# Kernel optimization log

Hardware: AMD Instinct MI355X
Metric: run time of the kernel (lower is better)

The kernel has to match this reference:

```python
import jax, jax.numpy as jnp
import numpy as np
import math

B, H, L, DK, D, LOCAL = 4, 8, 2048, 64, 512, 4


def setup_inputs() -> dict:
    key = jax.random.key(0)
    ks = jax.random.split(key, 9)
    n = L
    return {
        'query': jax.random.normal(ks[0], (B, H, L, DK), jnp.float32),
        'key': jax.random.normal(ks[1], (B, H, L, DK), jnp.float32),
        'value': jax.random.normal(ks[2], (B, H, L, DK), jnp.float32),
        'users': jax.random.normal(ks[3], (B, L, D), jnp.float32),
        'mask': jnp.tril(jnp.ones((L, L), dtype=bool))[None, None],  # causal [1,1,L,L]
        'rel_pos_w': jax.random.normal(ks[4], (2 * n - 1, DK * LOCAL), jnp.float32) * 0.02,
        'user_proj_w': jax.random.normal(ks[5], (DK * LOCAL, D), jnp.float32) * 0.02,
        'user_proj_b': jax.random.normal(ks[6], (DK * LOCAL,), jnp.float32) * 0.02,
        'mlp_w': jax.random.normal(ks[7], (LOCAL, DK), jnp.float32) * 0.1,
        'mlp_b': jax.random.normal(ks[8], (LOCAL,), jnp.float32) * 0.1,
    }


def reference(query, key, value, users, mask, rel_pos_w, user_proj_w, user_proj_b, mlp_w, mlp_b):
    b, h, l, dk = query.shape
    local = mlp_w.shape[0]
    g = h - local
    n = l
    scale = 1.0 / math.sqrt(dk)
    NEG = -1e12  # MAX_VAL in the torch source

    # ---- global heads: plain softmax attention ----
    qg, kg, vg = query[:, :g], key[:, :g], value[:, :g]
    sg = jnp.einsum('bhqd,bhkd->bhqk', qg, kg) * scale
    sg = jnp.where(mask, sg, NEG)
    pg = jax.nn.softmax(sg, axis=-1)
    og = jnp.einsum('bhqk,bhkd->bhqd', pg, vg)

    # ---- local (LOCKER) heads ----
    ql, kl, vl = query[:, g:], key[:, g:], value[:, g:]
    sl = jnp.einsum('bhqd,bhkd->bhqk', ql, kl) * scale

    # reweight = Linear(d_k,1)(rel_pos + v_q + v_k + user_proj(users)_q) per local head.
    # Linear over a sum decomposes exactly (same math, avoids [b,local,l,l,dk] tensor):
    rel_tab = rel_pos_w.reshape(2 * n - 1, local, dk)
    rel_scores = jnp.einsum('rhd,hd->rh', rel_tab, mlp_w)          # [2n-1, local]
    pos = jnp.arange(n)
    distance = pos[None, :] - pos[:, None] + n - 1                  # [l, l]
    rel_term = rel_scores[distance].transpose(2, 0, 1)              # [local, l, l]

    v_term = jnp.einsum('bhkd,hd->bhk', vl, mlp_w)                  # [b, local, l]
    u = (users @ user_proj_w.T + user_proj_b).reshape(b, l, local, dk)
    u_term = jnp.einsum('bqhd,hd->bhq', u, mlp_w)                   # [b, local, l]

    reweight = (rel_term[None]
                + v_term[:, :, None, :]      # value_l.unsqueeze(-3): varies over key idx
                + v_term[:, :, :, None]      # value_l.unsqueeze(-2): varies over query idx
                + u_term[:, :, :, None]      # user term broadcast over key idx
                + mlp_b[None, :, None, None])

    sl = sl + reweight
    sl = jnp.where(mask, sl, NEG)
    pl = jax.nn.softmax(sl, axis=-1)
    ol = jnp.einsum('bhqk,bhkd->bhqd', pl, vl)

    return jnp.concatenate([og, ol], axis=1)  # [b, h, l, d_k]
```

## Files before the change

### kernel.cpp

```cpp
#include <hip/hip_runtime.h>

#define TL 2048
#define NHEAD 8
#define NLOC 4
#define L2E 1.44269504f

typedef __attribute__((ext_vector_type(4))) float f32x4;
typedef __attribute__((ext_vector_type(8))) __bf16 bf16x8;
typedef __attribute__((ext_vector_type(4))) __bf16 bf16x4;
typedef __attribute__((ext_vector_type(8))) unsigned short u16x8;

static __device__ __forceinline__ unsigned short f2bf(float f) {
    unsigned u = __float_as_uint(f);
    u = (u + 0x7FFFu + ((u >> 16) & 1u)) >> 16;
    return (unsigned short)u;
}
static __device__ __forceinline__ float bf2f(unsigned short u) {
    return __uint_as_float(((unsigned)u) << 16);
}
static __device__ __forceinline__ void gl_lds16(const void* g, void* l) {
    __builtin_amdgcn_global_load_lds(
        (const __attribute__((address_space(1))) void*)g,
        (__attribute__((address_space(3))) void*)l, 16, 0, 0);
}

__global__ __launch_bounds__(256) void relscore_kernel(
    const float* __restrict__ rel_pos_w, const float* __restrict__ mlp_w,
    unsigned short* __restrict__ rel_sb) {
    int r = blockIdx.x;
    int t = threadIdx.x;
    int w = t >> 6, lane = t & 63;
    float v = rel_pos_w[r * 256 + t] * mlp_w[t];
#pragma unroll
    for (int off = 32; off; off >>= 1) v += __shfl_xor(v, off);
    if (lane == 0) rel_sb[w * 4096 + r] = f2bf(v * L2E);
}

__global__ __launch_bounds__(256) void preconv_kernel(
    const float* __restrict__ key, const float* __restrict__ value,
    const float* __restrict__ mlp_w,
    unsigned short* __restrict__ Kb, unsigned short* __restrict__ Vtb,
    unsigned short* __restrict__ vtb) {
    __shared__ float Vf[64][66];
    int blk = blockIdx.x;
    int t = threadIdx.x;
    int bh = blk >> 5, kt = blk & 31;
    int h = bh & 7, b = bh >> 3;
    size_t src = (size_t)blk * 4096;
    size_t dst = (size_t)blk * 4096;

#pragma unroll
    for (int i = 0; i < 2; ++i) {
        int ch = t + i * 256;
        int row = ch >> 3, c = ch & 7;
        const float* kp = key + src + row * 64 + c * 8;
        f32x4 a = *(const f32x4*)kp;
        f32x4 bb = *(const f32x4*)(kp + 4);
        u16x8 o;
#pragma unroll
        for (int j = 0; j < 4; ++j) { o[j] = f2bf(a[j]); o[4 + j] = f2bf(bb[j]); }
        *(u16x8*)&Kb[dst + row * 64 + ((c ^ (row & 7)) << 3)] = o;
    }
    {
        int row = t >> 2, q4 = t & 3;
        const float* vp = value + src + row * 64 + q4 * 16;
#pragma unroll
        for (int j = 0; j < 4; ++j)
            *(f32x4*)&Vf[row][q4 * 16 + j * 4] = *(const f32x4*)(vp + j * 4);
    }
    __syncthreads();
#pragma unroll
    for (int i = 0; i < 2; ++i) {
        int ch = t + i * 256;
        int dr = ch >> 3, c = ch & 7;
        u16x8 o;
#pragma unroll
        for (int j = 0; j < 8; ++j) o[j] = f2bf(Vf[c * 8 + j][dr]);
        *(u16x8*)&Vtb[dst + dr * 64 + ((c ^ (dr & 7)) << 3)] = o;
    }
    if (h >= NLOC) {
        int wave = t >> 6, lane = t & 63;
        float mw = mlp_w[(h - NLOC) * 64 + lane];
        unsigned short* vout = vtb + (size_t)((b * NLOC + h - NLOC) * TL) + kt * 64;
#pragma unroll
        for (int i = 0; i < 16; ++i) {
            int row = wave * 16 + i;
            float v = Vf[row][lane] * mw;
#pragma unroll
            for (int off = 32; off; off >>= 1) v += __shfl_xor(v, off);
            if (lane == 0) vout[row] = f2bf(v * L2E);
        }
    }
}

__global__ __launch_bounds__(256, 4) void attn_kernel(
    const float* __restrict__ query,
    const unsigned short* __restrict__ Kb, const unsigned short* __restrict__ Vtb,
    const unsigned short* __restrict__ rel_sb, const unsigned short* __restrict__ vtb,
    float* __restrict__ out) {

    __shared__ __align__(16) unsigned char smem[37248];
    unsigned short* Ks0  = (unsigned short*)smem;
    unsigned short* Vt0  = (unsigned short*)(smem + 16384);
    unsigned short* relb = (unsigned short*)(smem + 32768);
    unsigned short* bias0 = (unsigned short*)(smem + 36992);

    int bid = blockIdx.x;
    int qbi = bid >> 5;
    int bh = bid & 31;
    int qb = (qbi < 16) ? (31 - qbi) : (qbi - 16);
    int h = bh & 7;
    int b = bh >> 3;
    int q0 = qb << 6;
    int t = threadIdx.x;
    int wave = t >> 6, lane = t & 63;
    int l15 = lane & 15, l4 = lane >> 4;
    bool islocal = (h >= NLOC);

    size_t base = (size_t)bh * TL * 64;
    const unsigned short* Ktiles = Kb + (size_t)bh * 32 * 4096;
    const unsigned short* Vtiles = Vtb + (size_t)bh * 32 * 4096;
    const unsigned short* vtp =
        vtb + (islocal ? (size_t)((b * NLOC + h - NLOC) * TL) : 0);

    gl_lds16(Ktiles + t * 8, Ks0 + t * 8);
    gl_lds16(Ktiles + 2048 + t * 8, Ks0 + 2048 + t * 8);
    gl_lds16(Vtiles + t * 8, Vt0 + t * 8);
    gl_lds16(Vtiles + 2048 + t * 8, Vt0 + 2048 + t * 8);
    if (islocal) {
        const u16x8* src = (const u16x8*)(rel_sb + (h - NLOC) * 4096);
        u16x8* dst = (u16x8*)relb;
        dst[t] = src[t];
        if (t < 8) {
            dst[256 + t] = src[256 + t];
            *(u16x8*)&bias0[t * 8] = *(const u16x8*)&vtp[t * 8];
        }
    }

    int qt = q0 + wave * 16;
    int q = qt + l15;

    const float SC = 0.125f * L2E;
    bf16x8 qf0, qf1;
    {
        const float* qsrc = query + base + (size_t)q * 64 + l4 * 8;
        f32x4 a = *(const f32x4*)qsrc;
        f32x4 bb = *(const f32x4*)(qsrc + 4);
        f32x4 c = *(const f32x4*)(qsrc + 32);
        f32x4 d = *(const f32x4*)(qsrc + 36);
        u16x8 u0, u1;
#pragma unroll
        for (int j = 0; j < 4; ++j) {
            u0[j] = f2bf(a[j] * SC); u0[4 + j] = f2bf(bb[j] * SC);
            u1[j] = f2bf(c[j] * SC); u1[4 + j] = f2bf(d[j] * SC);
        }
        qf0 = __builtin_bit_cast(bf16x8, u0);
        qf1 = __builtin_bit_cast(bf16x8, u1);
    }

    float m = -1e30f, lsum = 0.0f;
    f32x4 acc0 = {0.f, 0.f, 0.f, 0.f};
    f32x4 acc1 = acc0, acc2 = acc0, acc3 = acc0;

    __syncthreads();

    int cur = 0;
    for (int kt = 0; kt <= qb; ++kt) {
        unsigned short* Ks = Ks0 + cur * 4096;
        unsigned short* Vt = Vt0 + cur * 4096;
        unsigned short* bias = bias0 + cur * 64;

        if (kt < qb) {
            int nb = cur ^ 1;
            const unsigned short* gk = Ktiles + (size_t)(kt + 1) * 4096;
            const unsigned short* gv = Vtiles + (size_t)(kt + 1) * 4096;
            gl_lds16(gk + t * 8, Ks0 + nb * 4096 + t * 8);
            gl_lds16(gk + 2048 + t * 8, Ks0 + nb * 4096 + 2048 + t * 8);
            gl_lds16(gv + t * 8, Vt0 + nb * 4096 + t * 8);
            gl_lds16(gv + 2048 + t * 8, Vt0 + nb * 4096 + 2048 + t * 8);
            if (islocal && t < 8)
                *(u16x8*)&bias0[nb * 64 + t * 8] =
                    *(const u16x8*)&vtp[(kt + 1) * 64 + t * 8];
        }

        int k0 = kt << 6;
        bool diag = (kt == qb);
        int s16max = diag ? wave : 3;

        f32x4 sfr[4];
#pragma unroll
        for (int s16 = 0; s16 < 4; ++s16) {
            if (s16 <= s16max) {
                int r = s16 * 16 + l15;
                int sw = r & 7;
                const bf16x8 kf0 = *(const bf16x8*)&Ks[r * 64 + ((l4 ^ sw) << 3)];
                const bf16x8 kf1 = *(const bf16x8*)&Ks[r * 64 + (((4 + l4) ^ sw) << 3)];
                f32x4 z = {0.f, 0.f, 0.f, 0.f};
                z = __builtin_amdgcn_mfma_f32_16x16x32_bf16(kf0, qf0, z, 0, 0, 0);
                z = __builtin_amdgcn_mfma_f32_16x16x32_bf16(kf1, qf1, z, 0, 0, 0);
                sfr[s16] = z;
            } else {
                sfr[s16] = (f32x4){-1e30f, -1e30f, -1e30f, -1e30f};
            }
        }

        float sv[16];
        float tmax = -1e30f;
#pragma unroll
        for (int s16 = 0; s16 < 4; ++s16) {
#pragma unroll
            for (int rg = 0; rg < 4; ++rg) {
                int kk = s16 * 16 + l4 * 4 + rg;
                int k = k0 + kk;
                float s = sfr[s16][rg];
                if (s16 <= s16max) {
                    if (islocal) s += bf2f(relb[k - q + 2047]) + bf2f(bias[kk]);
                    if (diag && k > q) s = -1e30f;
                }
                sv[s16 * 4 + rg] = s;
                tmax = fmaxf(tmax, s);
            }
        }
        tmax = fmaxf(tmax, __shfl_xor(tmax, 16));
        tmax = fmaxf(tmax, __shfl_xor(tmax, 32));
        if (__any(tmax > m + 11.5f)) {
            float newm = fmaxf(m, tmax);
            float corr = exp2f(m - newm);
            lsum *= corr;
            acc0 *= corr; acc1 *= corr; acc2 *= corr; acc3 *= corr;
            m = newm;
        }
        float psum = 0.f;
        bf16x4 pq[4];
#pragma unroll
        for (int s16 = 0; s16 < 4; ++s16) {
#pragma unroll
            for (int rg = 0; rg < 4; ++rg) {
                float p = exp2f(sv[s16 * 4 + rg] - m);
                psum += p;
                pq[s16][rg] = (__bf16)p;
            }
        }
        psum += __shfl_xor(psum, 16);
        psum += __shfl_xor(psum, 32);
        lsum += psum;

        asm volatile("s_waitcnt lgkmcnt(0)" ::: "memory");
        __builtin_amdgcn_s_barrier();
        __builtin_amdgcn_sched_barrier(0);

        unsigned short* Pw = Ks + wave * 1024;
#pragma unroll
        for (int s16 = 0; s16 < 4; ++s16) {
            int c = 2 * s16 + (l4 >> 1);
            *(unsigned long long*)&Pw[l15 * 64 + ((c ^ (l15 & 7)) << 3) + ((l4 & 1) << 2)] =
                __builtin_bit_cast(unsigned long long, pq[s16]);
        }

#pragma unroll
        for (int half = 0; half < 2; ++half) {
            const bf16x8 pf =
                *(const bf16x8*)&Pw[l15 * 64 + (((half * 4 + l4) ^ (l15 & 7)) << 3)];
            int cbase = half * 4 + l4;
#pragma unroll
            for (int dblk = 0; dblk < 4; ++dblk) {
                int r = dblk * 16 + l15;
                const bf16x8 vf =
                    *(const bf16x8*)&Vt[r * 64 + ((cbase ^ (r & 7)) << 3)];
                f32x4* ac = dblk == 0 ? &acc0 : dblk == 1 ? &acc1
                          : dblk == 2 ? &acc2 : &acc3;
                *ac = __builtin_amdgcn_mfma_f32_16x16x32_bf16(vf, pf, *ac, 0, 0, 0);
            }
        }

        __syncthreads();
        cur ^= 1;
    }

    float invl = 1.0f / lsum;
    float* ob = (float*)(smem + wave * 4352);
    *(f32x4*)&ob[l15 * 68 + 0  + l4 * 4] = acc0 * invl;
    *(f32x4*)&ob[l15 * 68 + 16 + l4 * 4] = acc1 * invl;
    *(f32x4*)&ob[l15 * 68 + 32 + l4 * 4] = acc2 * invl;
    *(f32x4*)&ob[l15 * 68 + 48 + l4 * 4] = acc3 * invl;
    size_t obase = base + (size_t)qt * 64;
#pragma unroll
    for (int it = 0; it < 4; ++it) {
        int row = lane >> 2;
        int col = (lane & 3) * 16 + it * 4;
        f32x4 o = *(const f32x4*)&ob[row * 68 + col];
        *(f32x4*)(out + obase + (size_t)row * 64 + col) = o;
    }
}

extern "C" void kernel_launch(void* const* d_in, const int* in_sizes, int n_in,
                              void* d_out, int out_size, void* d_ws, size_t ws_size,
                              hipStream_t stream) {
    const float* query = (const float*)d_in[0];
    const float* key = (const float*)d_in[1];
    const float* value = (const float*)d_in[2];
    const float* rel_pos_w = (const float*)d_in[5];
    const float* mlp_w = (const float*)d_in[8];
    float* out = (float*)d_out;

    unsigned short* Kb = (unsigned short*)d_ws;
    unsigned short* Vtb = Kb + 32 * 32 * 4096;
    unsigned short* rel_sb = Vtb + 32 * 32 * 4096;
    unsigned short* vtb = rel_sb + 4 * 4096;

    relscore_kernel<<<4095, 256, 0, stream>>>(rel_pos_w, mlp_w, rel_sb);
    preconv_kernel<<<1024, 256, 0, stream>>>(key, value, mlp_w, Kb, Vtb, vtb);
    attn_kernel<<<1024, 256, 0, stream>>>(query, Kb, Vtb, rel_sb, vtb, out);
}
```

Measured before the change: 88.95 us.

## Pair causal query blocks per workgroup and keep relative bias in fp32

Each workgroup now handles two query blocks (qb and 31-qb) of the same batch-head back to back, so every block runs 33 key tiles and the causal work is balanced. The grid is halved to 512 and the flash-attention state is flushed and reset between the two blocks. Relative-position scores and the per-key value bias are now stored in LDS as fp32 instead of bf16, which raises LDS use and lowers the occupancy hint to 2. The intent is to remove the causal load imbalance and the tail effect of the old grid, at the cost of fewer resident workgroups and more LDS per block.

```diff
diff --git a/kernel.cpp b/kernel.cpp
--- a/kernel.cpp
+++ b/kernel.cpp
@@ -26,14 +26,14 @@
 
 __global__ __launch_bounds__(256) void relscore_kernel(
     const float* __restrict__ rel_pos_w, const float* __restrict__ mlp_w,
-    unsigned short* __restrict__ rel_sb) {
+    float* __restrict__ rel_sf) {
     int r = blockIdx.x;
     int t = threadIdx.x;
     int w = t >> 6, lane = t & 63;
     float v = rel_pos_w[r * 256 + t] * mlp_w[t];
 #pragma unroll
     for (int off = 32; off; off >>= 1) v += __shfl_xor(v, off);
-    if (lane == 0) rel_sb[w * 4096 + r] = f2bf(v * L2E);
+    if (lane == 0) rel_sf[w * 4096 + r] = v * L2E;
 }
 
 __global__ __launch_bounds__(256) void preconv_kernel(
@@ -93,25 +93,25 @@
     }
 }
 
-__global__ __launch_bounds__(256, 4) void attn_kernel(
+__global__ __launch_bounds__(256, 2) void attn_kernel(
     const float* __restrict__ query,
     const unsigned short* __restrict__ Kb, const unsigned short* __restrict__ Vtb,
-    const unsigned short* __restrict__ rel_sb, const unsigned short* __restrict__ vtb,
+    const float* __restrict__ rel_sf, const unsigned short* __restrict__ vtb,
     float* __restrict__ out) {
 
-    __shared__ __align__(16) unsigned char smem[37248];
-    unsigned short* Ks0  = (unsigned short*)smem;
-    unsigned short* Vt0  = (unsigned short*)(smem + 16384);
-    unsigned short* relb = (unsigned short*)(smem + 32768);
-    unsigned short* bias0 = (unsigned short*)(smem + 36992);
+    __shared__ __align__(16) unsigned char smem[59136];
+    unsigned short* Ks0 = (unsigned short*)smem;
+    unsigned short* Vt0 = (unsigned short*)(smem + 16384);
+    float* relf  = (float*)(smem + 32768);
+    float* biasf = (float*)(smem + 41216);
+    float* epil  = (float*)(smem + 41728);
 
     int bid = blockIdx.x;
-    int qbi = bid >> 5;
-    int bh = bid & 31;
-    int qb = (qbi < 16) ? (31 - qbi) : (qbi - 16);
-    int h = bh & 7;
-    int b = bh >> 3;
-    int q0 = qb << 6;
+    int xslot = bid & 7, jj = bid >> 3;
+    int pair = jj >> 2, sub = jj & 3;
+    int bh = xslot * 4 + sub;
+    int qbA = 31 - pair, qbB = pair;
+    int h = bh & 7, b = bh >> 3;
     int t = threadIdx.x;
     int wave = t >> 6, lane = t & 63;
     int l15 = lane & 15, l4 = lane >> 4;
@@ -128,22 +128,17 @@
     gl_lds16(Vtiles + t * 8, Vt0 + t * 8);
     gl_lds16(Vtiles + 2048 + t * 8, Vt0 + 2048 + t * 8);
     if (islocal) {
-        const u16x8* src = (const u16x8*)(rel_sb + (h - NLOC) * 4096);
-        u16x8* dst = (u16x8*)relb;
+        const f32x4* src = (const f32x4*)(rel_sf + (h - NLOC) * 4096);
+        f32x4* dst = (f32x4*)relf;
         dst[t] = src[t];
-        if (t < 8) {
-            dst[256 + t] = src[256 + t];
-            *(u16x8*)&bias0[t * 8] = *(const u16x8*)&vtp[t * 8];
-        }
-    }
-
-    int qt = q0 + wave * 16;
-    int q = qt + l15;
+        dst[t + 256] = src[t + 256];
+        if (t < 16) dst[t + 512] = src[t + 512];
+        if (t < 64) biasf[t] = bf2f(vtp[t]);
+    }
 
     const float SC = 0.125f * L2E;
-    bf16x8 qf0, qf1;
-    {
-        const float* qsrc = query + base + (size_t)q * 64 + l4 * 8;
+    auto loadQ = [&](int qrow, bf16x8& f0, bf16x8& f1) {
+        const float* qsrc = query + base + (size_t)qrow * 64 + l4 * 8;
         f32x4 a = *(const f32x4*)qsrc;
         f32x4 bb = *(const f32x4*)(qsrc + 4);
         f32x4 c = *(const f32x4*)(qsrc + 32);
@@ -154,33 +149,66 @@
             u0[j] = f2bf(a[j] * SC); u0[4 + j] = f2bf(bb[j] * SC);
             u1[j] = f2bf(c[j] * SC); u1[4 + j] = f2bf(d[j] * SC);
         }
-        qf0 = __builtin_bit_cast(bf16x8, u0);
-        qf1 = __builtin_bit_cast(bf16x8, u1);
-    }
+        f0 = __builtin_bit_cast(bf16x8, u0);
+        f1 = __builtin_bit_cast(bf16x8, u1);
+    };
+
+    int qb = qbA;
+    int qt = (qbA << 6) + wave * 16;
+    int q = qt + l15;
+    bf16x8 qf0, qf1;
+    loadQ(q, qf0, qf1);
 
     float m = -1e30f, lsum = 0.0f;
     f32x4 acc0 = {0.f, 0.f, 0.f, 0.f};
     f32x4 acc1 = acc0, acc2 = acc0, acc3 = acc0;
 
+    auto flush = [&]() {
+        float invl = 1.0f / lsum;
+        float* ob = epil + wave * 1088;
+        *(f32x4*)&ob[l15 * 68 + 0  + l4 * 4] = acc0 * invl;
+        *(f32x4*)&ob[l15 * 68 + 16 + l4 * 4] = acc1 * invl;
+        *(f32x4*)&ob[l15 * 68 + 32 + l4 * 4] = acc2 * invl;
+        *(f32x4*)&ob[l15 * 68 + 48 + l4 * 4] = acc3 * invl;
+        size_t obase = base + (size_t)qt * 64;
+#pragma unroll
+        for (int it = 0; it < 4; ++it) {
+            int row = lane >> 2;
+            int col = (lane & 3) * 16 + it * 4;
+            f32x4 o = *(const f32x4*)&ob[row * 68 + col];
+            *(f32x4*)(out + obase + (size_t)row * 64 + col) = o;
+        }
+    };
+
     __syncthreads();
 
-    int cur = 0;
-    for (int kt = 0; kt <= qb; ++kt) {
+    int cur = 0, ktbase = 0;
+    for (int i = 0; i <= 32; ++i) {
+        if (i == qbA + 1) {
+            flush();
+            qb = qbB; ktbase = i;
+            qt = (qbB << 6) + wave * 16;
+            q = qt + l15;
+            loadQ(q, qf0, qf1);
+            m = -1e30f; lsum = 0.0f;
+            acc0 = (f32x4){0.f, 0.f, 0.f, 0.f};
+            acc1 = acc0; acc2 = acc0; acc3 = acc0;
+        }
+        int kt = i - ktbase;
         unsigned short* Ks = Ks0 + cur * 4096;
         unsigned short* Vt = Vt0 + cur * 4096;
-        unsigned short* bias = bias0 + cur * 64;
-
-        if (kt < qb) {
+        const float* bias = biasf + cur * 64;
+
+        if (i < 32) {
             int nb = cur ^ 1;
-            const unsigned short* gk = Ktiles + (size_t)(kt + 1) * 4096;
-            const unsigned short* gv = Vtiles + (size_t)(kt + 1) * 4096;
+            int nkt = (i + 1 <= qbA) ? (i + 1) : (i - qbA);
+            const unsigned short* gk = Ktiles + (size_t)nkt * 4096;
+            const unsigned short* gv = Vtiles + (size_t)nkt * 4096;
             gl_lds16(gk + t * 8, Ks0 + nb * 4096 + t * 8);
             gl_lds16(gk + 2048 + t * 8, Ks0 + nb * 4096 + 2048 + t * 8);
             gl_lds16(gv + t * 8, Vt0 + nb * 4096 + t * 8);
             gl_lds16(gv + 2048 + t * 8, Vt0 + nb * 4096 + 2048 + t * 8);
-            if (islocal && t < 8)
-                *(u16x8*)&bias0[nb * 64 + t * 8] =
-                    *(const u16x8*)&vtp[(kt + 1) * 64 + t * 8];
+            if (islocal && t < 64) biasf[nb * 64 + t] = bf2f(vtp[nkt * 64 + t]);
         }
 
         int k0 = kt << 6;
@@ -208,13 +236,15 @@
         float tmax = -1e30f;
 #pragma unroll
         for (int s16 = 0; s16 < 4; ++s16) {
+            f32x4 bv;
+            if (islocal) bv = *(const f32x4*)&bias[s16 * 16 + l4 * 4];
 #pragma unroll
             for (int rg = 0; rg < 4; ++rg) {
                 int kk = s16 * 16 + l4 * 4 + rg;
                 int k = k0 + kk;
                 float s = sfr[s16][rg];
                 if (s16 <= s16max) {
-                    if (islocal) s += bf2f(relb[k - q + 2047]) + bf2f(bias[kk]);
+                    if (islocal) s += relf[k - q + 2047] + bv[rg];
                     if (diag && k > q) s = -1e30f;
                 }
                 sv[s16 * 4 + rg] = s;
@@ -277,20 +307,7 @@
         cur ^= 1;
     }
 
-    float invl = 1.0f / lsum;
-    float* ob = (float*)(smem + wave * 4352);
-    *(f32x4*)&ob[l15 * 68 + 0  + l4 * 4] = acc0 * invl;
-    *(f32x4*)&ob[l15 * 68 + 16 + l4 * 4] = acc1 * invl;
-    *(f32x4*)&ob[l15 * 68 + 32 + l4 * 4] = acc2 * invl;
-    *(f32x4*)&ob[l15 * 68 + 48 + l4 * 4] = acc3 * invl;
-    size_t obase = base + (size_t)qt * 64;
-#pragma unroll
-    for (int it = 0; it < 4; ++it) {
-        int row = lane >> 2;
-        int col = (lane & 3) * 16 + it * 4;
-        f32x4 o = *(const f32x4*)&ob[row * 68 + col];
-        *(f32x4*)(out + obase + (size_t)row * 64 + col) = o;
-    }
+    flush();
 }
 
 extern "C" void kernel_launch(void* const* d_in, const int* in_sizes, int n_in,
@@ -305,10 +322,10 @@
 
     unsigned short* Kb = (unsigned short*)d_ws;
     unsigned short* Vtb = Kb + 32 * 32 * 4096;
-    unsigned short* rel_sb = Vtb + 32 * 32 * 4096;
-    unsigned short* vtb = rel_sb + 4 * 4096;
-
-    relscore_kernel<<<4095, 256, 0, stream>>>(rel_pos_w, mlp_w, rel_sb);
+    float* rel_sf = (float*)(Vtb + 32 * 32 * 4096);
+    unsigned short* vtb = (unsigned short*)(rel_sf + 4 * 4096);
+
+    relscore_kernel<<<4095, 256, 0, stream>>>(rel_pos_w, mlp_w, rel_sf);
     preconv_kernel<<<1024, 256, 0, stream>>>(key, value, mlp_w, Kb, Vtb, vtb);
-    attn_kernel<<<1024, 256, 0, stream>>>(query, Kb, Vtb, rel_sb, vtb, out);
-}
+    attn_kernel<<<512, 256, 0, stream>>>(query, Kb, Vtb, rel_sf, vtb, out);
+}
```

New measurement: 112.7 us. 1.27x slower.

## Split long causal query blocks across two workgroups and merge partials

Applied to the files above, without the earlier changes.

Query blocks 16-31, which have the longest causal key ranges, are now each split into two workgroups covering halves of the key range. Each half writes unnormalized accumulators plus running max and sum to a workspace, and a new merge kernel combines them. Short blocks still run as a single workgroup and now write output directly, without staging through LDS. This evens out per-workgroup work and improves tail balance, at the cost of an extra launch and partial-result traffic. The bias is also stored in LDS as fp32 and read as vectors.

```diff
diff --git a/kernel.cpp b/kernel.cpp
--- a/kernel.cpp
+++ b/kernel.cpp
@@ -4,6 +4,7 @@
 #define NHEAD 8
 #define NLOC 4
 #define L2E 1.44269504f
+#define PART_STRIDE 4224
 
 typedef __attribute__((ext_vector_type(4))) float f32x4;
 typedef __attribute__((ext_vector_type(8))) __bf16 bf16x8;
@@ -97,20 +98,37 @@
     const float* __restrict__ query,
     const unsigned short* __restrict__ Kb, const unsigned short* __restrict__ Vtb,
     const unsigned short* __restrict__ rel_sb, const unsigned short* __restrict__ vtb,
-    float* __restrict__ out) {
-
-    __shared__ __align__(16) unsigned char smem[37248];
-    unsigned short* Ks0  = (unsigned short*)smem;
-    unsigned short* Vt0  = (unsigned short*)(smem + 16384);
+    float* __restrict__ out, float* __restrict__ part) {
+
+    __shared__ __align__(16) unsigned char smem[37504];
+    unsigned short* Ks0 = (unsigned short*)smem;
+    unsigned short* Vt0 = (unsigned short*)(smem + 16384);
     unsigned short* relb = (unsigned short*)(smem + 32768);
-    unsigned short* bias0 = (unsigned short*)(smem + 36992);
+    float* biasf = (float*)(smem + 36992);
 
     int bid = blockIdx.x;
-    int qbi = bid >> 5;
-    int bh = bid & 31;
-    int qb = (qbi < 16) ? (31 - qbi) : (qbi - 16);
-    int h = bh & 7;
-    int b = bh >> 3;
+    int bh, qb, ktb, kte;
+    bool split;
+    float* ppart = nullptr;
+    if (bid < 1024) {
+        int qbi = bid >> 6;
+        qb = 31 - qbi;
+        int half = bid & 1;
+        bh = (bid >> 1) & 31;
+        int sA = (qb + 1) >> 1;
+        split = true;
+        if (half == 0) { ktb = 0; kte = sA - 1; }
+        else           { ktb = sA; kte = qb; }
+        ppart = part + (size_t)(((qb - 16) * 32 + bh) * 2 + half) * PART_STRIDE;
+    } else {
+        int s = bid - 1024;
+        qb = 15 - (s >> 5);
+        bh = s & 31;
+        ktb = 0; kte = qb;
+        split = false;
+    }
+
+    int h = bh & 7, b = bh >> 3;
     int q0 = qb << 6;
     int t = threadIdx.x;
     int wave = t >> 6, lane = t & 63;
@@ -123,18 +141,20 @@
     const unsigned short* vtp =
         vtb + (islocal ? (size_t)((b * NLOC + h - NLOC) * TL) : 0);
 
-    gl_lds16(Ktiles + t * 8, Ks0 + t * 8);
-    gl_lds16(Ktiles + 2048 + t * 8, Ks0 + 2048 + t * 8);
-    gl_lds16(Vtiles + t * 8, Vt0 + t * 8);
-    gl_lds16(Vtiles + 2048 + t * 8, Vt0 + 2048 + t * 8);
+    {
+        const unsigned short* gk = Ktiles + (size_t)ktb * 4096;
+        const unsigned short* gv = Vtiles + (size_t)ktb * 4096;
+        gl_lds16(gk + t * 8, Ks0 + t * 8);
+        gl_lds16(gk + 2048 + t * 8, Ks0 + 2048 + t * 8);
+        gl_lds16(gv + t * 8, Vt0 + t * 8);
+        gl_lds16(gv + 2048 + t * 8, Vt0 + 2048 + t * 8);
+    }
     if (islocal) {
         const u16x8* src = (const u16x8*)(rel_sb + (h - NLOC) * 4096);
         u16x8* dst = (u16x8*)relb;
         dst[t] = src[t];
-        if (t < 8) {
-            dst[256 + t] = src[256 + t];
-            *(u16x8*)&bias0[t * 8] = *(const u16x8*)&vtp[t * 8];
-        }
+        if (t < 8) dst[256 + t] = src[256 + t];
+        if (t < 64) biasf[t] = bf2f(vtp[ktb * 64 + t]);
     }
 
     int qt = q0 + wave * 16;
@@ -165,12 +185,12 @@
     __syncthreads();
 
     int cur = 0;
-    for (int kt = 0; kt <= qb; ++kt) {
+    for (int kt = ktb; kt <= kte; ++kt) {
         unsigned short* Ks = Ks0 + cur * 4096;
         unsigned short* Vt = Vt0 + cur * 4096;
-        unsigned short* bias = bias0 + cur * 64;
-
-        if (kt < qb) {
+        const float* bias = biasf + cur * 64;
+
+        if (kt < kte) {
             int nb = cur ^ 1;
             const unsigned short* gk = Ktiles + (size_t)(kt + 1) * 4096;
             const unsigned short* gv = Vtiles + (size_t)(kt + 1) * 4096;
@@ -178,9 +198,8 @@
             gl_lds16(gk + 2048 + t * 8, Ks0 + nb * 4096 + 2048 + t * 8);
             gl_lds16(gv + t * 8, Vt0 + nb * 4096 + t * 8);
             gl_lds16(gv + 2048 + t * 8, Vt0 + nb * 4096 + 2048 + t * 8);
-            if (islocal && t < 8)
-                *(u16x8*)&bias0[nb * 64 + t * 8] =
-                    *(const u16x8*)&vtp[(kt + 1) * 64 + t * 8];
+            if (islocal && t < 64)
+                biasf[nb * 64 + t] = bf2f(vtp[(kt + 1) * 64 + t]);
         }
 
         int k0 = kt << 6;
@@ -208,13 +227,15 @@
         float tmax = -1e30f;
 #pragma unroll
         for (int s16 = 0; s16 < 4; ++s16) {
+            f32x4 bv;
+            if (islocal) bv = *(const f32x4*)&bias[s16 * 16 + l4 * 4];
 #pragma unroll
             for (int rg = 0; rg < 4; ++rg) {
                 int kk = s16 * 16 + l4 * 4 + rg;
                 int k = k0 + kk;
                 float s = sfr[s16][rg];
                 if (s16 <= s16max) {
-                    if (islocal) s += bf2f(relb[k - q + 2047]) + bf2f(bias[kk]);
+                    if (islocal) s += bf2f(relb[k - q + 2047]) + bv[rg];
                     if (diag && k > q) s = -1e30f;
                 }
                 sv[s16 * 4 + rg] = s;
@@ -277,19 +298,49 @@
         cur ^= 1;
     }
 
-    float invl = 1.0f / lsum;
-    float* ob = (float*)(smem + wave * 4352);
-    *(f32x4*)&ob[l15 * 68 + 0  + l4 * 4] = acc0 * invl;
-    *(f32x4*)&ob[l15 * 68 + 16 + l4 * 4] = acc1 * invl;
-    *(f32x4*)&ob[l15 * 68 + 32 + l4 * 4] = acc2 * invl;
-    *(f32x4*)&ob[l15 * 68 + 48 + l4 * 4] = acc3 * invl;
-    size_t obase = base + (size_t)qt * 64;
-#pragma unroll
-    for (int it = 0; it < 4; ++it) {
-        int row = lane >> 2;
-        int col = (lane & 3) * 16 + it * 4;
-        f32x4 o = *(const f32x4*)&ob[row * 68 + col];
-        *(f32x4*)(out + obase + (size_t)row * 64 + col) = o;
+    if (split) {
+        int slot = wave * 256 + l4 * 16 + l15;
+        *(f32x4*)&ppart[(slot + 0)   * 4] = acc0;
+        *(f32x4*)&ppart[(slot + 64)  * 4] = acc1;
+        *(f32x4*)&ppart[(slot + 128) * 4] = acc2;
+        *(f32x4*)&ppart[(slot + 192) * 4] = acc3;
+        if (l4 == 0) {
+            ppart[4096 + wave * 16 + l15] = m;
+            ppart[4160 + wave * 16 + l15] = lsum;
+        }
+    } else {
+        float invl = 1.0f / lsum;
+        float* ob = out + base + (size_t)q * 64 + l4 * 4;
+        *(f32x4*)(ob + 0)  = acc0 * invl;
+        *(f32x4*)(ob + 16) = acc1 * invl;
+        *(f32x4*)(ob + 32) = acc2 * invl;
+        *(f32x4*)(ob + 48) = acc3 * invl;
+    }
+}
+
+__global__ __launch_bounds__(256) void merge_kernel(
+    const float* __restrict__ part, float* __restrict__ out) {
+    int bid = blockIdx.x;
+    int qb = 16 + (bid >> 5);
+    int bh = bid & 31;
+    const float* pA = part + (size_t)(((qb - 16) * 32 + bh) * 2) * PART_STRIDE;
+    const float* pB = pA + PART_STRIDE;
+    int t = threadIdx.x;
+    int q = t >> 2, ds4 = t & 3;
+    float ma = pA[4096 + q], la = pA[4160 + q];
+    float mb = pB[4096 + q], lb = pB[4160 + q];
+    float nm = fmaxf(ma, mb);
+    float ca = exp2f(ma - nm), cb = exp2f(mb - nm);
+    float inv = 1.0f / (la * ca + lb * cb);
+    ca *= inv; cb *= inv;
+    int s0 = ((q >> 4) * 256 + ds4 * 64 + (q & 15)) * 4;
+    size_t obase = ((size_t)bh * TL + qb * 64 + q) * 64 + ds4 * 16;
+#pragma unroll
+    for (int j4 = 0; j4 < 4; ++j4) {
+        f32x4 a = *(const f32x4*)&pA[s0 + j4 * 64];
+        f32x4 b = *(const f32x4*)&pB[s0 + j4 * 64];
+        f32x4 o = a * ca + b * cb;
+        *(f32x4*)(out + obase + j4 * 4) = o;
     }
 }
 
@@ -307,8 +358,10 @@
     unsigned short* Vtb = Kb + 32 * 32 * 4096;
     unsigned short* rel_sb = Vtb + 32 * 32 * 4096;
     unsigned short* vtb = rel_sb + 4 * 4096;
+    float* part = (float*)(vtb + 32 * 2048);
 
     relscore_kernel<<<4095, 256, 0, stream>>>(rel_pos_w, mlp_w, rel_sb);
     preconv_kernel<<<1024, 256, 0, stream>>>(key, value, mlp_w, Kb, Vtb, vtb);
-    attn_kernel<<<1024, 256, 0, stream>>>(query, Kb, Vtb, rel_sb, vtb, out);
-}
+    attn_kernel<<<1536, 256, 0, stream>>>(query, Kb, Vtb, rel_sb, vtb, out, part);
+    merge_kernel<<<512, 256, 0, stream>>>(part, out);
+}
```

Result: slower. 104.7 us (+17.7%).

## Split attention over key chunks with 32x32 MFMA and separate merge kernel

Applied to the files above, without the earlier changes.

Restructures the attention kernel so each block handles 256 queries (8 waves of 32) over a chunk of up to 6 key tiles, with 864 blocks balanced across causal lengths. It switches to 32x32x16 bf16 MFMA, keeps P in registers via lane shuffles instead of an LDS round trip, and stores rel/bias terms as fp32. Partial outputs (bf16) plus max/sum go to a workspace and a new merge kernel combines them. This adds an extra kernel launch and partial-output traffic, and storing partials in bf16 costs some precision.

```diff
diff --git a/kernel.cpp b/kernel.cpp
--- a/kernel.cpp
+++ b/kernel.cpp
@@ -4,19 +4,23 @@
 #define NHEAD 8
 #define NLOC 4
 #define L2E 1.44269504f
+#define PSTRIDE 8704
 
 typedef __attribute__((ext_vector_type(4))) float f32x4;
+typedef __attribute__((ext_vector_type(16))) float f32x16;
 typedef __attribute__((ext_vector_type(8))) __bf16 bf16x8;
-typedef __attribute__((ext_vector_type(4))) __bf16 bf16x4;
 typedef __attribute__((ext_vector_type(8))) unsigned short u16x8;
+typedef __attribute__((ext_vector_type(4))) unsigned int u32x4;
 
 static __device__ __forceinline__ unsigned short f2bf(float f) {
     unsigned u = __float_as_uint(f);
     u = (u + 0x7FFFu + ((u >> 16) & 1u)) >> 16;
     return (unsigned short)u;
 }
-static __device__ __forceinline__ float bf2f(unsigned short u) {
-    return __uint_as_float(((unsigned)u) << 16);
+static __device__ __forceinline__ unsigned int cvtpk(float a, float b) {
+    unsigned int w;
+    asm("v_cvt_pk_bf16_f32 %0, %1, %2" : "=v"(w) : "v"(a), "v"(b));
+    return w;
 }
 static __device__ __forceinline__ void gl_lds16(const void* g, void* l) {
     __builtin_amdgcn_global_load_lds(
@@ -26,21 +30,21 @@
 
 __global__ __launch_bounds__(256) void relscore_kernel(
     const float* __restrict__ rel_pos_w, const float* __restrict__ mlp_w,
-    unsigned short* __restrict__ rel_sb) {
+    float* __restrict__ rel_sf) {
     int r = blockIdx.x;
     int t = threadIdx.x;
     int w = t >> 6, lane = t & 63;
     float v = rel_pos_w[r * 256 + t] * mlp_w[t];
 #pragma unroll
     for (int off = 32; off; off >>= 1) v += __shfl_xor(v, off);
-    if (lane == 0) rel_sb[w * 4096 + r] = f2bf(v * L2E);
+    if (lane == 0) rel_sf[w * 4096 + r] = v * L2E;
 }
 
 __global__ __launch_bounds__(256) void preconv_kernel(
     const float* __restrict__ key, const float* __restrict__ value,
     const float* __restrict__ mlp_w,
     unsigned short* __restrict__ Kb, unsigned short* __restrict__ Vtb,
-    unsigned short* __restrict__ vtb) {
+    float* __restrict__ vtbf) {
     __shared__ float Vf[64][66];
     int blk = blockIdx.x;
     int t = threadIdx.x;
@@ -81,215 +85,276 @@
     if (h >= NLOC) {
         int wave = t >> 6, lane = t & 63;
         float mw = mlp_w[(h - NLOC) * 64 + lane];
-        unsigned short* vout = vtb + (size_t)((b * NLOC + h - NLOC) * TL) + kt * 64;
+        float* vout = vtbf + (size_t)((b * NLOC + h - NLOC) * TL) + kt * 64;
 #pragma unroll
         for (int i = 0; i < 16; ++i) {
             int row = wave * 16 + i;
             float v = Vf[row][lane] * mw;
 #pragma unroll
             for (int off = 32; off; off >>= 1) v += __shfl_xor(v, off);
-            if (lane == 0) vout[row] = f2bf(v * L2E);
-        }
-    }
-}
-
-__global__ __launch_bounds__(256, 4) void attn_kernel(
+            if (lane == 0) vout[row] = v * L2E;
+        }
+    }
+}
+
+#define MFMA32(A, B, C) __builtin_amdgcn_mfma_f32_32x32x16_bf16(A, B, C, 0, 0, 0)
+#define SV(h2) ((h2) ? S1 : S0)
+#define OV(dh) ((dh) ? O1 : O0)
+
+__global__ __launch_bounds__(512, 4) void attn_kernel(
     const float* __restrict__ query,
     const unsigned short* __restrict__ Kb, const unsigned short* __restrict__ Vtb,
-    const unsigned short* __restrict__ rel_sb, const unsigned short* __restrict__ vtb,
-    float* __restrict__ out) {
-
-    __shared__ __align__(16) unsigned char smem[37248];
-    unsigned short* Ks0  = (unsigned short*)smem;
-    unsigned short* Vt0  = (unsigned short*)(smem + 16384);
-    unsigned short* relb = (unsigned short*)(smem + 32768);
-    unsigned short* bias0 = (unsigned short*)(smem + 36992);
+    const float* __restrict__ rel_sf, const float* __restrict__ vtbf,
+    float* __restrict__ part) {
+
+    __shared__ __align__(16) unsigned char smem[35840];
+    unsigned short* Ks0 = (unsigned short*)smem;
+    unsigned short* Vt0 = (unsigned short*)(smem + 16384);
+    float* relw  = (float*)(smem + 32768);
+    float* biasf = (float*)(smem + 35328);
 
     int bid = blockIdx.x;
-    int qbi = bid >> 5;
     int bh = bid & 31;
-    int qb = (qbi < 16) ? (31 - qbi) : (qbi - 16);
-    int h = bh & 7;
-    int b = bh >> 3;
-    int q0 = qb << 6;
+    int sid = bid >> 5;
+    int i, sb;
+    if (sid < 6)       { i = 7; sb = 0; }
+    else if (sid < 11) { i = 6; sb = 6; }
+    else if (sid < 15) { i = 5; sb = 11; }
+    else if (sid < 19) { i = 4; sb = 15; }
+    else if (sid < 22) { i = 3; sb = 19; }
+    else if (sid < 24) { i = 2; sb = 22; }
+    else if (sid < 26) { i = 1; sb = 24; }
+    else               { i = 0; sb = 26; }
+    int s = sid - sb;
+    int k_b = 6 * s;
+    int k_e = min(6 * s + 6, 4 * i + 4);
+    int q0 = i << 8;
+
+    int h = bh & 7, b = bh >> 3;
+    bool islocal = (h >= NLOC);
     int t = threadIdx.x;
-    int wave = t >> 6, lane = t & 63;
-    int l15 = lane & 15, l4 = lane >> 4;
-    bool islocal = (h >= NLOC);
-
-    size_t base = (size_t)bh * TL * 64;
-    const unsigned short* Ktiles = Kb + (size_t)bh * 32 * 4096;
-    const unsigned short* Vtiles = Vtb + (size_t)bh * 32 * 4096;
-    const unsigned short* vtp =
-        vtb + (islocal ? (size_t)((b * NLOC + h - NLOC) * TL) : 0);
-
-    gl_lds16(Ktiles + t * 8, Ks0 + t * 8);
-    gl_lds16(Ktiles + 2048 + t * 8, Ks0 + 2048 + t * 8);
-    gl_lds16(Vtiles + t * 8, Vt0 + t * 8);
-    gl_lds16(Vtiles + 2048 + t * 8, Vt0 + 2048 + t * 8);
+    int w = t >> 6;
+    int l31 = t & 31;
+    int hi = (t >> 5) & 1;
+    int sw = l31 & 7;
+    int qrel = 32 * w + l31;
+    int qglob = q0 + qrel;
+    int qmaxw = q0 + 32 * w + 31;
+
+    size_t tbase = (size_t)bh * 32 * 4096;
+    const unsigned short* Ktiles = Kb + tbase;
+    const unsigned short* Vtiles = Vtb + tbase;
+    const float* vtpf = vtbf + (islocal ? (size_t)((b * NLOC + h - NLOC) * TL) : 0);
+    int idxlo = 64 * k_b - q0 + 1792;
+    const float* relsrc = rel_sf + (islocal ? ((h - NLOC) * 4096 + idxlo) : 0);
+
+    gl_lds16(Ktiles + (size_t)k_b * 4096 + t * 8, Ks0 + t * 8);
+    gl_lds16(Vtiles + (size_t)k_b * 4096 + t * 8, Vt0 + t * 8);
     if (islocal) {
-        const u16x8* src = (const u16x8*)(rel_sb + (h - NLOC) * 4096);
-        u16x8* dst = (u16x8*)relb;
-        dst[t] = src[t];
-        if (t < 8) {
-            dst[256 + t] = src[256 + t];
-            *(u16x8*)&bias0[t * 8] = *(const u16x8*)&vtp[t * 8];
-        }
-    }
-
-    int qt = q0 + wave * 16;
-    int q = qt + l15;
+        if (t < 160) *((f32x4*)relw + t) = *((const f32x4*)relsrc + t);
+        if (t < 16) ((f32x4*)biasf)[t] = ((const f32x4*)(vtpf + (size_t)k_b * 64))[t];
+    }
 
     const float SC = 0.125f * L2E;
-    bf16x8 qf0, qf1;
+    bf16x8 qf[4];
     {
-        const float* qsrc = query + base + (size_t)q * 64 + l4 * 8;
-        f32x4 a = *(const f32x4*)qsrc;
-        f32x4 bb = *(const f32x4*)(qsrc + 4);
-        f32x4 c = *(const f32x4*)(qsrc + 32);
-        f32x4 d = *(const f32x4*)(qsrc + 36);
-        u16x8 u0, u1;
-#pragma unroll
-        for (int j = 0; j < 4; ++j) {
-            u0[j] = f2bf(a[j] * SC); u0[4 + j] = f2bf(bb[j] * SC);
-            u1[j] = f2bf(c[j] * SC); u1[4 + j] = f2bf(d[j] * SC);
-        }
-        qf0 = __builtin_bit_cast(bf16x8, u0);
-        qf1 = __builtin_bit_cast(bf16x8, u1);
-    }
-
-    float m = -1e30f, lsum = 0.0f;
-    f32x4 acc0 = {0.f, 0.f, 0.f, 0.f};
-    f32x4 acc1 = acc0, acc2 = acc0, acc3 = acc0;
+        const float* qsrc = query + ((size_t)bh * TL + qglob) * 64 + 8 * hi;
+#pragma unroll
+        for (int mq = 0; mq < 4; ++mq) {
+            f32x4 a = *(const f32x4*)(qsrc + 16 * mq);
+            f32x4 c = *(const f32x4*)(qsrc + 16 * mq + 4);
+            u16x8 u;
+#pragma unroll
+            for (int j = 0; j < 4; ++j) { u[j] = f2bf(a[j] * SC); u[4 + j] = f2bf(c[j] * SC); }
+            qf[mq] = __builtin_bit_cast(bf16x8, u);
+        }
+    }
+
+    float m = -1e30f, lsum = 0.f;
+    f32x16 O0 = {0,0,0,0,0,0,0,0,0,0,0,0,0,0,0,0};
+    f32x16 O1 = {0,0,0,0,0,0,0,0,0,0,0,0,0,0,0,0};
 
     __syncthreads();
 
     int cur = 0;
-    for (int kt = 0; kt <= qb; ++kt) {
+    for (int kt = k_b; kt < k_e; ++kt) {
         unsigned short* Ks = Ks0 + cur * 4096;
         unsigned short* Vt = Vt0 + cur * 4096;
-        unsigned short* bias = bias0 + cur * 64;
-
-        if (kt < qb) {
+        const float* bias = biasf + cur * 64;
+
+        if (kt + 1 < k_e) {
             int nb = cur ^ 1;
-            const unsigned short* gk = Ktiles + (size_t)(kt + 1) * 4096;
-            const unsigned short* gv = Vtiles + (size_t)(kt + 1) * 4096;
-            gl_lds16(gk + t * 8, Ks0 + nb * 4096 + t * 8);
-            gl_lds16(gk + 2048 + t * 8, Ks0 + nb * 4096 + 2048 + t * 8);
-            gl_lds16(gv + t * 8, Vt0 + nb * 4096 + t * 8);
-            gl_lds16(gv + 2048 + t * 8, Vt0 + nb * 4096 + 2048 + t * 8);
-            if (islocal && t < 8)
-                *(u16x8*)&bias0[nb * 64 + t * 8] =
-                    *(const u16x8*)&vtp[(kt + 1) * 64 + t * 8];
-        }
-
-        int k0 = kt << 6;
-        bool diag = (kt == qb);
-        int s16max = diag ? wave : 3;
-
-        f32x4 sfr[4];
-#pragma unroll
-        for (int s16 = 0; s16 < 4; ++s16) {
-            if (s16 <= s16max) {
-                int r = s16 * 16 + l15;
-                int sw = r & 7;
-                const bf16x8 kf0 = *(const bf16x8*)&Ks[r * 64 + ((l4 ^ sw) << 3)];
-                const bf16x8 kf1 = *(const bf16x8*)&Ks[r * 64 + (((4 + l4) ^ sw) << 3)];
-                f32x4 z = {0.f, 0.f, 0.f, 0.f};
-                z = __builtin_amdgcn_mfma_f32_16x16x32_bf16(kf0, qf0, z, 0, 0, 0);
-                z = __builtin_amdgcn_mfma_f32_16x16x32_bf16(kf1, qf1, z, 0, 0, 0);
-                sfr[s16] = z;
-            } else {
-                sfr[s16] = (f32x4){-1e30f, -1e30f, -1e30f, -1e30f};
-            }
-        }
-
-        float sv[16];
-        float tmax = -1e30f;
-#pragma unroll
-        for (int s16 = 0; s16 < 4; ++s16) {
-#pragma unroll
-            for (int rg = 0; rg < 4; ++rg) {
-                int kk = s16 * 16 + l4 * 4 + rg;
-                int k = k0 + kk;
-                float s = sfr[s16][rg];
-                if (s16 <= s16max) {
-                    if (islocal) s += bf2f(relb[k - q + 2047]) + bf2f(bias[kk]);
-                    if (diag && k > q) s = -1e30f;
+            gl_lds16(Ktiles + (size_t)(kt + 1) * 4096 + t * 8, Ks0 + nb * 4096 + t * 8);
+            gl_lds16(Vtiles + (size_t)(kt + 1) * 4096 + t * 8, Vt0 + nb * 4096 + t * 8);
+            if (islocal && t < 16)
+                ((f32x4*)(biasf + nb * 64))[t] =
+                    ((const f32x4*)(vtpf + (size_t)(kt + 1) * 64))[t];
+        }
+
+        bool active = (64 * kt <= qmaxw);
+        if (active) {
+            f32x16 S0 = {0,0,0,0,0,0,0,0,0,0,0,0,0,0,0,0};
+            f32x16 S1 = {0,0,0,0,0,0,0,0,0,0,0,0,0,0,0,0};
+#pragma unroll
+            for (int mq = 0; mq < 4; ++mq) {
+                int ch = ((2 * mq + hi) ^ sw) << 3;
+                const bf16x8 kf0 = *(const bf16x8*)&Ks[l31 * 64 + ch];
+                const bf16x8 kf1 = *(const bf16x8*)&Ks[(32 + l31) * 64 + ch];
+                S0 = MFMA32(kf0, qf[mq], S0);
+                S1 = MFMA32(kf1, qf[mq], S1);
+            }
+
+            if (islocal) {
+                int rbase = 64 * (kt - k_b) + 255 - qrel;
+#pragma unroll
+                for (int h2 = 0; h2 < 2; ++h2)
+#pragma unroll
+                    for (int g = 0; g < 4; ++g) {
+                        int kk0 = 32 * h2 + 8 * g + 4 * hi;
+                        f32x4 bv = *(const f32x4*)&bias[kk0];
+                        int ro = rbase + kk0;
+#pragma unroll
+                        for (int j = 0; j < 4; ++j)
+                            SV(h2)[4 * g + j] += bv[j] + relw[ro + j];
+                    }
+            }
+            if (64 * kt + 63 > q0 + 32 * w) {
+                int koff = 64 * kt - qglob;
+#pragma unroll
+                for (int h2 = 0; h2 < 2; ++h2)
+#pragma unroll
+                    for (int r = 0; r < 16; ++r) {
+                        int kk = 32 * h2 + (r & 3) + 8 * (r >> 2) + 4 * hi;
+                        if (koff + kk > 0) SV(h2)[r] = -1e30f;
+                    }
+            }
+            float pmax = -1e30f;
+#pragma unroll
+            for (int r = 0; r < 16; ++r) pmax = fmaxf(pmax, fmaxf(S0[r], S1[r]));
+            pmax = fmaxf(pmax, __shfl_xor(pmax, 32));
+            if (__any(pmax > m + 11.5f)) {
+                float nm2 = fmaxf(m, pmax);
+                float corr = exp2f(m - nm2);
+                lsum *= corr;
+#pragma unroll
+                for (int r = 0; r < 16; ++r) { O0[r] *= corr; O1[r] *= corr; }
+                m = nm2;
+            }
+            float ps = 0.f;
+#pragma unroll
+            for (int r = 0; r < 16; ++r) {
+                float p0 = exp2f(S0[r] - m), p1 = exp2f(S1[r] - m);
+                S0[r] = p0; S1[r] = p1; ps += p0 + p1;
+            }
+            ps += __shfl_xor(ps, 32);
+            lsum += ps;
+
+#pragma unroll
+            for (int kq = 0; kq < 4; ++kq) {
+                int ra = (kq & 1) ? 8 : 0;
+                unsigned int x0, x1, y0, y1;
+                if (kq & 2) {
+                    x0 = cvtpk(S1[ra + 0], S1[ra + 1]); x1 = cvtpk(S1[ra + 2], S1[ra + 3]);
+                    y0 = cvtpk(S1[ra + 4], S1[ra + 5]); y1 = cvtpk(S1[ra + 6], S1[ra + 7]);
+                } else {
+                    x0 = cvtpk(S0[ra + 0], S0[ra + 1]); x1 = cvtpk(S0[ra + 2], S0[ra + 3]);
+                    y0 = cvtpk(S0[ra + 4], S0[ra + 5]); y1 = cvtpk(S0[ra + 6], S0[ra + 7]);
                 }
-                sv[s16 * 4 + rg] = s;
-                tmax = fmaxf(tmax, s);
-            }
-        }
-        tmax = fmaxf(tmax, __shfl_xor(tmax, 16));
-        tmax = fmaxf(tmax, __shfl_xor(tmax, 32));
-        if (__any(tmax > m + 11.5f)) {
-            float newm = fmaxf(m, tmax);
-            float corr = exp2f(m - newm);
-            lsum *= corr;
-            acc0 *= corr; acc1 *= corr; acc2 *= corr; acc3 *= corr;
-            m = newm;
-        }
-        float psum = 0.f;
-        bf16x4 pq[4];
-#pragma unroll
-        for (int s16 = 0; s16 < 4; ++s16) {
-#pragma unroll
-            for (int rg = 0; rg < 4; ++rg) {
-                float p = exp2f(sv[s16 * 4 + rg] - m);
-                psum += p;
-                pq[s16][rg] = (__bf16)p;
-            }
-        }
-        psum += __shfl_xor(psum, 16);
-        psum += __shfl_xor(psum, 32);
-        lsum += psum;
-
-        asm volatile("s_waitcnt lgkmcnt(0)" ::: "memory");
-        __builtin_amdgcn_s_barrier();
-        __builtin_amdgcn_sched_barrier(0);
-
-        unsigned short* Pw = Ks + wave * 1024;
-#pragma unroll
-        for (int s16 = 0; s16 < 4; ++s16) {
-            int c = 2 * s16 + (l4 >> 1);
-            *(unsigned long long*)&Pw[l15 * 64 + ((c ^ (l15 & 7)) << 3) + ((l4 & 1) << 2)] =
-                __builtin_bit_cast(unsigned long long, pq[s16]);
-        }
-
-#pragma unroll
-        for (int half = 0; half < 2; ++half) {
-            const bf16x8 pf =
-                *(const bf16x8*)&Pw[l15 * 64 + (((half * 4 + l4) ^ (l15 & 7)) << 3)];
-            int cbase = half * 4 + l4;
-#pragma unroll
-            for (int dblk = 0; dblk < 4; ++dblk) {
-                int r = dblk * 16 + l15;
-                const bf16x8 vf =
-                    *(const bf16x8*)&Vt[r * 64 + ((cbase ^ (r & 7)) << 3)];
-                f32x4* ac = dblk == 0 ? &acc0 : dblk == 1 ? &acc1
-                          : dblk == 2 ? &acc2 : &acc3;
-                *ac = __builtin_amdgcn_mfma_f32_16x16x32_bf16(vf, pf, *ac, 0, 0, 0);
-            }
-        }
-
+                unsigned int sx0 = __shfl_xor(x0, 32), sx1 = __shfl_xor(x1, 32);
+                unsigned int sy0 = __shfl_xor(y0, 32), sy1 = __shfl_xor(y1, 32);
+                u32x4 fw;
+                fw[0] = hi ? sy0 : x0;
+                fw[1] = hi ? sy1 : x1;
+                fw[2] = hi ? y0 : sx0;
+                fw[3] = hi ? y1 : sx1;
+                const bf16x8 pf = __builtin_bit_cast(bf16x8, fw);
+                int ch = ((2 * kq + hi) ^ sw) << 3;
+                const bf16x8 vf0 = *(const bf16x8*)&Vt[l31 * 64 + ch];
+                const bf16x8 vf1 = *(const bf16x8*)&Vt[(32 + l31) * 64 + ch];
+                O0 = MFMA32(vf0, pf, O0);
+                O1 = MFMA32(vf1, pf, O1);
+            }
+        }
         __syncthreads();
         cur ^= 1;
     }
 
-    float invl = 1.0f / lsum;
-    float* ob = (float*)(smem + wave * 4352);
-    *(f32x4*)&ob[l15 * 68 + 0  + l4 * 4] = acc0 * invl;
-    *(f32x4*)&ob[l15 * 68 + 16 + l4 * 4] = acc1 * invl;
-    *(f32x4*)&ob[l15 * 68 + 32 + l4 * 4] = acc2 * invl;
-    *(f32x4*)&ob[l15 * 68 + 48 + l4 * 4] = acc3 * invl;
-    size_t obase = base + (size_t)qt * 64;
-#pragma unroll
-    for (int it = 0; it < 4; ++it) {
-        int row = lane >> 2;
-        int col = (lane & 3) * 16 + it * 4;
-        f32x4 o = *(const f32x4*)&ob[row * 68 + col];
-        *(f32x4*)(out + obase + (size_t)row * 64 + col) = o;
+    float* pp = part + (size_t)bid * PSTRIDE;
+    unsigned int* po = (unsigned int*)pp;
+#pragma unroll
+    for (int g = 0; g < 4; ++g) {
+        unsigned int w0 = cvtpk(O0[4 * g + 0], O0[4 * g + 1]);
+        unsigned int w1 = cvtpk(O0[4 * g + 2], O0[4 * g + 3]);
+        unsigned int w2 = cvtpk(O1[4 * g + 0], O1[4 * g + 1]);
+        unsigned int w3 = cvtpk(O1[4 * g + 2], O1[4 * g + 3]);
+        int dp0 = 4 * g + 2 * hi;
+        po[dp0 * 256 + qrel] = w0;
+        po[(dp0 + 1) * 256 + qrel] = w1;
+        po[(16 + dp0) * 256 + qrel] = w2;
+        po[(16 + dp0 + 1) * 256 + qrel] = w3;
+    }
+    if (hi == 0) { pp[8192 + qrel] = m; pp[8448 + qrel] = lsum; }
+}
+
+__global__ __launch_bounds__(256) void merge_kernel(
+    const float* __restrict__ part, float* __restrict__ out) {
+    __shared__ float sc[6][256];
+    int bid = blockIdx.x;
+    int bh = bid & 31, i = bid >> 5;
+    int n, sb;
+    if (i == 7)      { n = 6; sb = 0; }
+    else if (i == 6) { n = 5; sb = 6; }
+    else if (i == 5) { n = 4; sb = 11; }
+    else if (i == 4) { n = 4; sb = 15; }
+    else if (i == 3) { n = 3; sb = 19; }
+    else if (i == 2) { n = 2; sb = 22; }
+    else if (i == 1) { n = 2; sb = 24; }
+    else             { n = 1; sb = 26; }
+    int t = threadIdx.x;
+
+    float mv[6], lv[6];
+#pragma unroll
+    for (int s2 = 0; s2 < 6; ++s2) {
+        mv[s2] = -1e30f; lv[s2] = 0.f;
+        if (s2 < n) {
+            const float* pp = part + (size_t)((sb + s2) * 32 + bh) * PSTRIDE;
+            mv[s2] = pp[8192 + t]; lv[s2] = pp[8448 + t];
+        }
+    }
+    float nm = mv[0];
+#pragma unroll
+    for (int s2 = 1; s2 < 6; ++s2) nm = fmaxf(nm, mv[s2]);
+    float den = 0.f;
+    float cf[6];
+#pragma unroll
+    for (int s2 = 0; s2 < 6; ++s2) { cf[s2] = exp2f(mv[s2] - nm); den += lv[s2] * cf[s2]; }
+    float inv = 1.0f / den;
+#pragma unroll
+    for (int s2 = 0; s2 < 6; ++s2) if (s2 < n) sc[s2][t] = cf[s2] * inv;
+    __syncthreads();
+
+    size_t obase = (size_t)bh * TL * 64 + (size_t)(256 * i + t) * 64;
+    for (int seg = 0; seg < 4; ++seg) {
+        float o[16];
+#pragma unroll
+        for (int j = 0; j < 16; ++j) o[j] = 0.f;
+#pragma unroll
+        for (int s2 = 0; s2 < 6; ++s2) {
+            if (s2 < n) {
+                const unsigned int* po =
+                    (const unsigned int*)(part + (size_t)((sb + s2) * 32 + bh) * PSTRIDE);
+                float wsc = sc[s2][t];
+#pragma unroll
+                for (int j = 0; j < 8; ++j) {
+                    unsigned int wv = po[(seg * 8 + j) * 256 + t];
+                    o[2 * j]     += wsc * __uint_as_float((wv & 0xffffu) << 16);
+                    o[2 * j + 1] += wsc * __uint_as_float(wv & 0xffff0000u);
+                }
+            }
+        }
+#pragma unroll
+        for (int c = 0; c < 4; ++c)
+            *(f32x4*)(out + obase + seg * 16 + 4 * c) = *(const f32x4*)&o[4 * c];
     }
 }
 
@@ -305,10 +370,12 @@
 
     unsigned short* Kb = (unsigned short*)d_ws;
     unsigned short* Vtb = Kb + 32 * 32 * 4096;
-    unsigned short* rel_sb = Vtb + 32 * 32 * 4096;
-    unsigned short* vtb = rel_sb + 4 * 4096;
-
-    relscore_kernel<<<4095, 256, 0, stream>>>(rel_pos_w, mlp_w, rel_sb);
-    preconv_kernel<<<1024, 256, 0, stream>>>(key, value, mlp_w, Kb, Vtb, vtb);
-    attn_kernel<<<1024, 256, 0, stream>>>(query, Kb, Vtb, rel_sb, vtb, out);
-}
+    float* rel_sf = (float*)(Vtb + 32 * 32 * 4096);
+    float* vtbf = rel_sf + 4 * 4096;
+    float* part = vtbf + 32768;
+
+    relscore_kernel<<<4095, 256, 0, stream>>>(rel_pos_w, mlp_w, rel_sf);
+    preconv_kernel<<<1024, 256, 0, stream>>>(key, value, mlp_w, Kb, Vtb, vtbf);
+    attn_kernel<<<864, 512, 0, stream>>>(query, Kb, Vtb, rel_sf, vtbf, part);
+    merge_kernel<<<256, 256, 0, stream>>>(part, out);
+}
```

New measurement: 167.7 us. +88.6%, slower.
